# Kernel optimization log

Hardware: AMD Instinct MI355X
Metric: run time of the kernel (lower is better)

Reference implementation:

```python
import jax, jax.numpy as jnp
import numpy as np

C = 256
GROUPS = 32
EPS = 1e-5


def setup_inputs() -> dict:
    key = jax.random.key(0)
    ks = jax.random.split(key, 7)
    B, D, H, W = 2, 8, 48, 48
    x = jax.random.normal(ks[0], (B, C, D, H, W), dtype=jnp.float32)
    norm_w = jnp.ones((C,), jnp.float32)
    norm_b = jnp.zeros((C,), jnp.float32)
    qkv_w = jax.random.normal(ks[1], (3 * C, C), jnp.float32) * (1.0 / np.sqrt(C))
    qkv_b = jnp.zeros((3 * C,), jnp.float32)
    proj_w = jax.random.normal(ks[2], (C, C), jnp.float32) * (1.0 / np.sqrt(C))
    proj_b = jnp.zeros((C,), jnp.float32)
    return {"x": x, "norm_w": norm_w, "norm_b": norm_b,
            "qkv_w": qkv_w, "qkv_b": qkv_b,
            "proj_w": proj_w, "proj_b": proj_b}


def _group_norm(x, w, b):
    B, Cc, D, H, Wd = x.shape
    xg = x.reshape(B, GROUPS, Cc // GROUPS, D, H, Wd)
    mu = xg.mean(axis=(2, 3, 4, 5), keepdims=True)
    var = xg.var(axis=(2, 3, 4, 5), keepdims=True)
    xn = ((xg - mu) * jax.lax.rsqrt(var + EPS)).reshape(B, Cc, D, H, Wd)
    return xn * w[None, :, None, None, None] + b[None, :, None, None, None]


def reference(x, norm_w, norm_b, qkv_w, qkv_b, proj_w, proj_b):
    Cc = x.shape[1]
    h = _group_norm(x, norm_w, norm_b)
    # 1x1x1 conv == channel matmul
    qkv = jnp.einsum('oc,bcdhw->bodhw', qkv_w, h) + qkv_b[None, :, None, None, None]
    q, k, v = jnp.split(qkv, 3, axis=1)
    scale = (Cc // 8) ** (-0.5)
    # [B, D, h, w, H, W] dense spatial attention per depth slice
    attn = jnp.einsum('bcdhw,bcdHW->bdhwHW', q * scale, k)
    # NOTE: original code softmaxes over the LAST axis only (W), not (H,W) jointly.
    attn = jax.nn.softmax(attn, axis=-1)
    out = jnp.einsum('bdhwHW,bcdHW->bcdhw', attn, v)
    out = jnp.einsum('oc,bcdhw->bodhw', proj_w, out) + proj_b[None, :, None, None, None]
    return x + out
```

## Files before the change

kernel.cpp:

```cpp
#include <hip/hip_runtime.h>
#include <hip/hip_bf16.h>

typedef __attribute__((ext_vector_type(8))) short short8;
typedef __attribute__((ext_vector_type(4))) float f32x4;
typedef __attribute__((ext_vector_type(16))) float f32x16;
typedef __attribute__((ext_vector_type(4))) unsigned int u32x4;
typedef unsigned int u32;
typedef unsigned short u16;

#define C_ 256
#define G_ 32
#define ND_ 18432
#define HW_ 2304
#define EPS_ 1e-5f
#define QS2_ 0.25503487f

static __device__ __forceinline__ u16 f2bf(float f) {
  __hip_bfloat16 h = __float2bfloat16(f);
  return __builtin_bit_cast(u16, h);
}

static __device__ __forceinline__ void gll16(const void* g, void* l) {
  __builtin_amdgcn_global_load_lds(
      (const __attribute__((address_space(1))) unsigned int*)g,
      (__attribute__((address_space(3))) unsigned int*)l, 16, 0, 0);
}

__global__ void k_convert_w(const float* __restrict__ qkv_w,
                            const float* __restrict__ proj_w,
                            u16* __restrict__ wout,
                            float* __restrict__ raw) {
  if (blockIdx.x == 0 && threadIdx.x < 128) raw[threadIdx.x] = 0.f;
  int i = blockIdx.x * 256 + threadIdx.x;
  if (i < 196608) wout[i] = f2bf(qkv_w[i]);
  else            wout[i] = f2bf(proj_w[i - 196608]);
}

__global__ __launch_bounds__(256) void k_gn_part(const float* __restrict__ x,
                                                 float* __restrict__ raw) {
  int grp = blockIdx.x >> 2, sub = blockIdx.x & 3;
  const float4* p = (const float4*)(x + (size_t)grp * 147456 + sub * 36864);
  float s1 = 0.f, s2 = 0.f;
  for (int i = threadIdx.x; i < 9216; i += 256) {
    float4 v = p[i];
    s1 += v.x + v.y + v.z + v.w;
    s2 += v.x*v.x + v.y*v.y + v.z*v.z + v.w*v.w;
  }
  for (int off = 1; off < 64; off <<= 1) {
    s1 += __shfl_xor(s1, off, 64);
    s2 += __shfl_xor(s2, off, 64);
  }
  __shared__ float a1[4], a2[4];
  int w = threadIdx.x >> 6;
  if ((threadIdx.x & 63) == 0) { a1[w] = s1; a2[w] = s2; }
  __syncthreads();
  if (threadIdx.x == 0) {
    float t1 = a1[0] + a1[1] + a1[2] + a1[3];
    float t2 = a2[0] + a2[1] + a2[2] + a2[3];
    atomicAdd(&raw[grp * 2], t1);
    atomicAdd(&raw[grp * 2 + 1], t2);
  }
}

__global__ void k_gn_fin(const float* __restrict__ raw, float* __restrict__ stats) {
  int g = threadIdx.x;
  if (g < 64) {
    float mu  = raw[g * 2] / 147456.0f;
    float var = raw[g * 2 + 1] / 147456.0f - mu * mu;
    stats[g * 2]     = mu;
    stats[g * 2 + 1] = rsqrtf(var + EPS_);
  }
}

__global__ __launch_bounds__(256) void k_tnorm(const float* __restrict__ x,
                                               const float* __restrict__ stats,
                                               const float* __restrict__ nw,
                                               const float* __restrict__ nb,
                                               u16* __restrict__ h_t) {
  __shared__ u16 tl[64 * 66];
  int wg = blockIdx.x;
  int nt = wg % 288; int ct = (wg / 288) & 3; int b = wg / 1152;
  int c0 = ct * 64, n0 = nt * 64;
  int tid = threadIdx.x;
#pragma unroll
  for (int p = 0; p < 4; p++) {
    int c_l = p * 16 + (tid >> 4);
    int n4  = (tid & 15) * 4;
    int cg  = c0 + c_l;
    float4 v = *(const float4*)(x + ((size_t)(b * C_ + cg)) * ND_ + n0 + n4);
    float mu = stats[(b * G_ + (cg >> 3)) * 2];
    float rs = stats[(b * G_ + (cg >> 3)) * 2 + 1];
    float w = nw[cg], bia = nb[cg];
    tl[(n4 + 0) * 66 + c_l] = f2bf((v.x - mu) * rs * w + bia);
    tl[(n4 + 1) * 66 + c_l] = f2bf((v.y - mu) * rs * w + bia);
    tl[(n4 + 2) * 66 + c_l] = f2bf((v.z - mu) * rs * w + bia);
    tl[(n4 + 3) * 66 + c_l] = f2bf((v.w - mu) * rs * w + bia);
  }
  __syncthreads();
#pragma unroll
  for (int p = 0; p < 2; p++) {
    int idx = p * 256 + tid;
    int n_l = idx >> 3, c8 = idx & 7;
    const u32* s = (const u32*)((const char*)tl + n_l * 132 + c8 * 16);
    uint4 vv; vv.x = s[0]; vv.y = s[1]; vv.z = s[2]; vv.w = s[3];
    *(uint4*)(h_t + ((size_t)(b * ND_ + n0 + n_l)) * C_ + c0 + c8 * 8) = vv;
  }
}

__global__ __launch_bounds__(256) void k_qk(const u16* __restrict__ h_t,
                                            const u16* __restrict__ w_qkv,
                                            const float* __restrict__ qkv_b,
                                            u16* __restrict__ q_ws,
                                            u16* __restrict__ k_ws) {
  int wg = blockIdx.x;
  int nt = wg % 288; int ot = (wg / 288) & 3; int b = wg / 1152;
  int n0 = nt * 64, o0 = ot * 128;
  int lane = threadIdx.x & 63; int w = threadIdx.x >> 6;
  int g = lane >> 4, lid = lane & 15;
  int n_w = n0 + w * 16;
  f32x4 acc[8];
#pragma unroll
  for (int t = 0; t < 8; t++) acc[t] = (f32x4){0.f, 0.f, 0.f, 0.f};
  const short8* Ab = (const short8*)(h_t + ((size_t)(b * ND_ + n_w + lid)) * C_ + g * 8);
#pragma unroll
  for (int ks = 0; ks < 8; ks++) {
    short8 a = Ab[ks * 4];
#pragma unroll
    for (int t = 0; t < 8; t++) {
      short8 bf = *(const short8*)(w_qkv + ((size_t)(o0 + t * 16 + lid)) * C_ + ks * 32 + g * 8);
      acc[t] = __builtin_amdgcn_mfma_f32_16x16x32_bf16(a, bf, acc[t], 0, 0, 0);
    }
  }
  if (o0 < 256) {
#pragma unroll
    for (int t = 0; t < 8; t++) {
      int o_t = o0 + t * 16;
      float bias = qkv_b[o_t + lid];
#pragma unroll
      for (int r = 0; r < 4; r++) {
        int n_idx = n_w + g * 4 + r;
        q_ws[((size_t)(b * ND_ + n_idx)) * C_ + o_t + lid] = f2bf((acc[t][r] + bias) * QS2_);
      }
    }
  } else {
#pragma unroll
    for (int t = 0; t < 8; t++) {
      int o_t = o0 + t * 16;
      float bias = qkv_b[o_t + lid];
      int oc = o_t - 256 + lid;
#pragma unroll
      for (int r = 0; r < 4; r++) {
        int n_idx = n_w + g * 4 + r;
        int dd = n_idx / 2304, hw = n_idx % 2304;
        int tt = hw / 48, kk = hw % 48;
        size_t off = ((size_t)((b * 8 + dd) * 48 + tt) * 1536 + (oc >> 3) * 48 + kk) * 8 + (oc & 7);
        k_ws[off] = f2bf(acc[t][r] + bias);
      }
    }
  }
}

__global__ __launch_bounds__(256) void k_v(const u16* __restrict__ h_t,
                                           const u16* __restrict__ w_qkv,
                                           const float* __restrict__ qkv_b,
                                           u16* __restrict__ v_ws) {
  int wg = blockIdx.x;
  int nt = wg % 144; int ot = (wg / 144) & 3; int b = wg / 576;
  int n0 = nt * 128, o0 = ot * 64;
  int lane = threadIdx.x & 63; int w = threadIdx.x >> 6;
  int g = lane >> 4, lid = lane & 15;
  int o_w = o0 + w * 16;
  f32x4 acc[8];
#pragma unroll
  for (int t = 0; t < 8; t++) acc[t] = (f32x4){0.f, 0.f, 0.f, 0.f};
  const short8* Ab = (const short8*)(w_qkv + ((size_t)(512 + o_w + lid)) * C_ + g * 8);
#pragma unroll
  for (int ks = 0; ks < 8; ks++) {
    short8 a = Ab[ks * 4];
#pragma unroll
    for (int t = 0; t < 8; t++) {
      short8 bf = *(const short8*)(h_t + ((size_t)(b * ND_ + n0 + t * 16 + lid)) * C_ + ks * 32 + g * 8);
      acc[t] = __builtin_amdgcn_mfma_f32_16x16x32_bf16(a, bf, acc[t], 0, 0, 0);
    }
  }
#pragma unroll
  for (int t = 0; t < 8; t++) {
#pragma unroll
    for (int r = 0; r < 4; r++) {
      int o = o_w + g * 4 + r;
      int n = n0 + t * 16 + lid;
      int d = n / 2304; int hw = n % 2304;
      int grp = hw / 48; int j = hw % 48;
      size_t idx = ((size_t)(((b * 8 + d) * 48 + grp) * 6 + (j >> 3))) * 2048 + o * 8 + (j & 7);
      v_ws[idx] = f2bf(acc[t][r] + qkv_b[512 + o]);
    }
  }
}

__global__ __launch_bounds__(256, 2) void k_attn(const u16* __restrict__ q_ws,
                                                 const u16* __restrict__ k_ws,
                                                 const u16* __restrict__ v_ws,
                                                 u16* __restrict__ ao) {
  __shared__ __align__(16) unsigned char lds[74240];
  int wg = blockIdx.x;
  int virt = (wg & 7) * 36 + (wg >> 3);
  int slice = virt / 18;
  int qt = virt % 18;
  int b = slice >> 3, d = slice & 7;
  int tid = threadIdx.x;
  int lane = tid & 63, w = tid >> 6;
  int l31 = lane & 31, hi = lane >> 5;

  const char* kgb = (const char*)k_ws + (size_t)slice * 1179648;
  const char* vgb = (const char*)v_ws + (size_t)slice * 1179648;

  size_t nbase = (size_t)b * ND_ + d * HW_ + qt * 128 + w * 32;
  const char* qp = (const char*)q_ws + (nbase + l31) * 512 + hi * 16;
  short8 qf[16];
#pragma unroll
  for (int ks = 0; ks < 16; ks++) qf[ks] = *(const short8*)(qp + ks * 32);

  f32x16 acc[8];
#pragma unroll
  for (int i = 0; i < 8; i++) acc[i] = (f32x16)0.0f;

#define STG_K(t_, base_) {                                             \
    const char* s_ = kgb + (size_t)(t_) * 24576 + tid * 16;            \
    char* d_ = (char*)lds + (base_) + w * 1024;                        \
    _Pragma("unroll")                                                  \
    for (int i_ = 0; i_ < 6; i_++)                                     \
      gll16(s_ + i_ * 4096, d_ + i_ * 4096);                           \
  }
#define STG_V(t_) {                                                    \
    const char* s_ = vgb + (size_t)(t_) * 24576 + tid * 16;            \
    char* d_ = (char*)lds + 49152 + w * 1024;                          \
    _Pragma("unroll")                                                  \
    for (int i_ = 0; i_ < 6; i_++)                                     \
      gll16(s_ + i_ * 4096, d_ + i_ * 4096);                           \
  }

  STG_K(0, 0);
  STG_V(0);
  __builtin_amdgcn_sched_barrier(0);
  asm volatile("s_waitcnt vmcnt(0)" ::: "memory");
  __builtin_amdgcn_sched_barrier(0);
  __builtin_amdgcn_s_barrier();

  int kcur = 0;
  for (int t = 0; t < 48; t++) {
    if (t < 47) STG_K(t + 1, (kcur ^ 1) * 24576);

    const char* kb = (const char*)lds + kcur * 24576;

    f32x16 S0 = (f32x16)0.0f, S1 = (f32x16)0.0f;
#pragma unroll
    for (int ks = 0; ks < 16; ks++) {
      const char* p = kb + (ks * 2 + hi) * 768 + l31 * 16;
      short8 k0 = *(const short8*)(p);
      short8 k1 = *(const short8*)(p + 512);
      S0 = __builtin_amdgcn_mfma_f32_32x32x16_bf16(k0, qf[ks], S0, 0, 0, 0);
      S1 = __builtin_amdgcn_mfma_f32_32x32x16_bf16(k1, qf[ks], S1, 0, 0, 0);
    }

#pragma unroll
    for (int r = 0; r < 16; r++) S0[r] = __builtin_amdgcn_exp2f(S0[r]);
#pragma unroll
    for (int r = 0; r < 8; r++)  S1[r] = __builtin_amdgcn_exp2f(S1[r]);
    float z = 0.f;
#pragma unroll
    for (int r = 0; r < 16; r++) z += S0[r];
#pragma unroll
    for (int r = 0; r < 8; r++)  z += S1[r];
    z += __shfl_xor(z, 32, 64);
    float inv = __builtin_amdgcn_rcpf(z);
#pragma unroll
    for (int r = 0; r < 16; r++) S0[r] *= inv;
#pragma unroll
    for (int r = 0; r < 8; r++)  S1[r] *= inv;

    short8 pa[3];
#pragma unroll
    for (int s = 0; s < 3; s++) {
      const f32x16& P = (s < 2) ? S0 : S1;
      const int a = (s == 1) ? 8 : 0;
      u32 u0, u1, v0, v1;
      asm("v_cvt_pk_bf16_f32 %0, %1, %2" : "=v"(u0) : "v"(P[a + 0]), "v"(P[a + 1]));
      asm("v_cvt_pk_bf16_f32 %0, %1, %2" : "=v"(u1) : "v"(P[a + 2]), "v"(P[a + 3]));
      asm("v_cvt_pk_bf16_f32 %0, %1, %2" : "=v"(v0) : "v"(P[a + 4]), "v"(P[a + 5]));
      asm("v_cvt_pk_bf16_f32 %0, %1, %2" : "=v"(v1) : "v"(P[a + 6]), "v"(P[a + 7]));
      asm("v_permlane32_swap_b32 %0, %1" : "+v"(u0), "+v"(v0));
      asm("v_permlane32_swap_b32 %0, %1" : "+v"(u1), "+v"(v1));
      u32x4 wv; wv[0] = u0; wv[1] = u1; wv[2] = v0; wv[3] = v1;
      pa[s] = __builtin_bit_cast(short8, wv);
    }

    __builtin_amdgcn_sched_barrier(0);
    asm volatile("s_waitcnt vmcnt(0)" ::: "memory");
    __builtin_amdgcn_sched_barrier(0);
    __builtin_amdgcn_s_barrier();

    const char* vb = (const char*)lds + 49152;
#pragma unroll
    for (int s = 0; s < 3; s++) {
      const char* vs = vb + (s * 2 + hi) * 4096 + l31 * 16;
#pragma unroll
      for (int ct = 0; ct < 8; ct++) {
        short8 vf = *(const short8*)(vs + ct * 512);
        acc[ct] = __builtin_amdgcn_mfma_f32_32x32x16_bf16(pa[s], vf, acc[ct], 0, 0, 0);
      }
    }

    __builtin_amdgcn_s_barrier();
    if (t < 47) STG_V(t + 1);
    kcur ^= 1;
  }

#pragma unroll
  for (int ct = 0; ct < 8; ct++) {
#pragma unroll
    for (int r = 0; r < 16; r++) {
      int ql = (r & 3) + 8 * (r >> 2) + 4 * hi;
      ao[(nbase + ql) * 256 + ct * 32 + l31] = f2bf(acc[ct][r]);
    }
  }
}

__global__ __launch_bounds__(256) void k_proj(const u16* __restrict__ ao,
                                              const u16* __restrict__ w_p,
                                              const float* __restrict__ proj_b,
                                              const float* __restrict__ x,
                                              float* __restrict__ out) {
  int wg = blockIdx.x;
  int nt = wg % 144; int ot = (wg / 144) & 3; int b = wg / 576;
  int n0 = nt * 128, o0 = ot * 64;
  int lane = threadIdx.x & 63; int w = threadIdx.x >> 6;
  int g = lane >> 4, lid = lane & 15;
  int o_w = o0 + w * 16;
  f32x4 acc[8];
#pragma unroll
  for (int t = 0; t < 8; t++) acc[t] = (f32x4){0.f, 0.f, 0.f, 0.f};
  const short8* Ab = (const short8*)(w_p + ((size_t)(o_w + lid)) * C_ + g * 8);
#pragma unroll
  for (int ks = 0; ks < 8; ks++) {
    short8 a = Ab[ks * 4];
#pragma unroll
    for (int t = 0; t < 8; t++) {
      short8 bf = *(const short8*)(ao + ((size_t)(b * ND_ + n0 + t * 16 + lid)) * C_ + ks * 32 + g * 8);
      acc[t] = __builtin_amdgcn_mfma_f32_16x16x32_bf16(a, bf, acc[t], 0, 0, 0);
    }
  }
#pragma unroll
  for (int t = 0; t < 8; t++) {
#pragma unroll
    for (int r = 0; r < 4; r++) {
      int o = o_w + g * 4 + r;
      size_t off = ((size_t)(b * C_ + o)) * ND_ + n0 + t * 16 + lid;
      out[off] = acc[t][r] + proj_b[o] + x[off];
    }
  }
}

extern "C" void kernel_launch(void* const* d_in, const int* in_sizes, int n_in,
                              void* d_out, int out_size, void* d_ws, size_t ws_size,
                              hipStream_t stream) {
  const float* x      = (const float*)d_in[0];
  const float* norm_w = (const float*)d_in[1];
  const float* norm_b = (const float*)d_in[2];
  const float* qkv_w  = (const float*)d_in[3];
  const float* qkv_b  = (const float*)d_in[4];
  const float* proj_w = (const float*)d_in[5];
  const float* proj_b = (const float*)d_in[6];

  char* ws = (char*)d_ws;
  float* stats = (float*)ws;
  float* raw   = (float*)(ws + 512);
  u16* w_qkv = (u16*)(ws + 1024);
  u16* w_p   = (u16*)(ws + 1024 + 393216);
  u16* h_t   = (u16*)(ws + 525312);
  u16* q_ws  = h_t + 9437184;
  u16* k_ws  = q_ws + 9437184;
  u16* v_ws  = k_ws + 9437184;
  u16* ao    = h_t;
  float* out = (float*)d_out;

  if (ws_size < (size_t)525312 + 4ull * 9437184ull * 2ull) return;

  hipLaunchKernelGGL(k_convert_w, dim3(1024), dim3(256), 0, stream, qkv_w, proj_w, w_qkv, raw);
  hipLaunchKernelGGL(k_gn_part,   dim3(256),  dim3(256), 0, stream, x, raw);
  hipLaunchKernelGGL(k_gn_fin,    dim3(1),    dim3(64),  0, stream, raw, stats);
  hipLaunchKernelGGL(k_tnorm,     dim3(2304), dim3(256), 0, stream, x, stats, norm_w, norm_b, h_t);
  hipLaunchKernelGGL(k_qk,        dim3(2304), dim3(256), 0, stream, h_t, w_qkv, qkv_b, q_ws, k_ws);
  hipLaunchKernelGGL(k_v,         dim3(1152), dim3(256), 0, stream, h_t, w_qkv, qkv_b, v_ws);
  hipLaunchKernelGGL(k_attn,      dim3(288),  dim3(256), 0, stream, q_ws, k_ws, v_ws, ao);
  hipLaunchKernelGGL(k_proj,      dim3(1152), dim3(256), 0, stream, ao, w_p, proj_b, x, out);
}
```

Baseline: 335.4 us.

## Process two query tiles per wave in attention to reuse K/V staging

Each wave in the attention kernel now computes two 32-row query tiles against each staged K/V tile, so each workgroup covers 256 queries and the grid halves from 288 to 144 blocks. Every K and V fragment read from LDS feeds twice as many MFMAs, and total global K/V staging traffic is halved. The cost is doubled accumulator and Q register use, which forces occupancy down to one block per CU. With 144 blocks on a 256-CU part, many CUs sit idle, trading parallelism for reuse.

```diff
diff --git a/kernel.cpp b/kernel.cpp
--- a/kernel.cpp
+++ b/kernel.cpp
@@ -197,15 +197,15 @@
   }
 }
 
-__global__ __launch_bounds__(256, 2) void k_attn(const u16* __restrict__ q_ws,
+__global__ __launch_bounds__(256, 1) void k_attn(const u16* __restrict__ q_ws,
                                                  const u16* __restrict__ k_ws,
                                                  const u16* __restrict__ v_ws,
                                                  u16* __restrict__ ao) {
-  __shared__ __align__(16) unsigned char lds[74240];
+  __shared__ __align__(16) unsigned char lds[84480];
   int wg = blockIdx.x;
-  int virt = (wg & 7) * 36 + (wg >> 3);
-  int slice = virt / 18;
-  int qt = virt % 18;
+  int virt = (wg & 7) * 18 + (wg >> 3);
+  int slice = virt / 9;
+  int qt = virt % 9;
   int b = slice >> 3, d = slice & 7;
   int tid = threadIdx.x;
   int lane = tid & 63, w = tid >> 6;
@@ -214,15 +214,17 @@
   const char* kgb = (const char*)k_ws + (size_t)slice * 1179648;
   const char* vgb = (const char*)v_ws + (size_t)slice * 1179648;
 
-  size_t nbase = (size_t)b * ND_ + d * HW_ + qt * 128 + w * 32;
-  const char* qp = (const char*)q_ws + (nbase + l31) * 512 + hi * 16;
-  short8 qf[16];
-#pragma unroll
-  for (int ks = 0; ks < 16; ks++) qf[ks] = *(const short8*)(qp + ks * 32);
-
-  f32x16 acc[8];
-#pragma unroll
-  for (int i = 0; i < 8; i++) acc[i] = (f32x16)0.0f;
+  size_t nbase = (size_t)b * ND_ + d * HW_ + qt * 256 + w * 64;
+  const char* qpA = (const char*)q_ws + (nbase + l31) * 512 + hi * 16;
+  const char* qpB = qpA + 32 * 512;
+  short8 qfa[16], qfb[16];
+#pragma unroll
+  for (int ks = 0; ks < 16; ks++) { qfa[ks] = *(const short8*)(qpA + ks * 32);
+                                    qfb[ks] = *(const short8*)(qpB + ks * 32); }
+
+  f32x16 accA[8], accB[8];
+#pragma unroll
+  for (int i = 0; i < 8; i++) { accA[i] = (f32x16)0.0f; accB[i] = (f32x16)0.0f; }
 
 #define STG_K(t_, base_) {                                             \
     const char* s_ = kgb + (size_t)(t_) * 24576 + tid * 16;            \
@@ -252,46 +254,54 @@
 
     const char* kb = (const char*)lds + kcur * 24576;
 
-    f32x16 S0 = (f32x16)0.0f, S1 = (f32x16)0.0f;
+    f32x16 S0a = (f32x16)0.0f, S1a = (f32x16)0.0f;
+    f32x16 S0b = (f32x16)0.0f, S1b = (f32x16)0.0f;
 #pragma unroll
     for (int ks = 0; ks < 16; ks++) {
       const char* p = kb + (ks * 2 + hi) * 768 + l31 * 16;
       short8 k0 = *(const short8*)(p);
       short8 k1 = *(const short8*)(p + 512);
-      S0 = __builtin_amdgcn_mfma_f32_32x32x16_bf16(k0, qf[ks], S0, 0, 0, 0);
-      S1 = __builtin_amdgcn_mfma_f32_32x32x16_bf16(k1, qf[ks], S1, 0, 0, 0);
-    }
-
-#pragma unroll
-    for (int r = 0; r < 16; r++) S0[r] = __builtin_amdgcn_exp2f(S0[r]);
-#pragma unroll
-    for (int r = 0; r < 8; r++)  S1[r] = __builtin_amdgcn_exp2f(S1[r]);
-    float z = 0.f;
-#pragma unroll
-    for (int r = 0; r < 16; r++) z += S0[r];
-#pragma unroll
-    for (int r = 0; r < 8; r++)  z += S1[r];
-    z += __shfl_xor(z, 32, 64);
-    float inv = __builtin_amdgcn_rcpf(z);
-#pragma unroll
-    for (int r = 0; r < 16; r++) S0[r] *= inv;
-#pragma unroll
-    for (int r = 0; r < 8; r++)  S1[r] *= inv;
-
-    short8 pa[3];
-#pragma unroll
-    for (int s = 0; s < 3; s++) {
-      const f32x16& P = (s < 2) ? S0 : S1;
-      const int a = (s == 1) ? 8 : 0;
-      u32 u0, u1, v0, v1;
-      asm("v_cvt_pk_bf16_f32 %0, %1, %2" : "=v"(u0) : "v"(P[a + 0]), "v"(P[a + 1]));
-      asm("v_cvt_pk_bf16_f32 %0, %1, %2" : "=v"(u1) : "v"(P[a + 2]), "v"(P[a + 3]));
-      asm("v_cvt_pk_bf16_f32 %0, %1, %2" : "=v"(v0) : "v"(P[a + 4]), "v"(P[a + 5]));
-      asm("v_cvt_pk_bf16_f32 %0, %1, %2" : "=v"(v1) : "v"(P[a + 6]), "v"(P[a + 7]));
-      asm("v_permlane32_swap_b32 %0, %1" : "+v"(u0), "+v"(v0));
-      asm("v_permlane32_swap_b32 %0, %1" : "+v"(u1), "+v"(v1));
-      u32x4 wv; wv[0] = u0; wv[1] = u1; wv[2] = v0; wv[3] = v1;
-      pa[s] = __builtin_bit_cast(short8, wv);
+      S0a = __builtin_amdgcn_mfma_f32_32x32x16_bf16(k0, qfa[ks], S0a, 0, 0, 0);
+      S0b = __builtin_amdgcn_mfma_f32_32x32x16_bf16(k0, qfb[ks], S0b, 0, 0, 0);
+      S1a = __builtin_amdgcn_mfma_f32_32x32x16_bf16(k1, qfa[ks], S1a, 0, 0, 0);
+      S1b = __builtin_amdgcn_mfma_f32_32x32x16_bf16(k1, qfb[ks], S1b, 0, 0, 0);
+    }
+
+    short8 paA[3], paB[3];
+#pragma unroll
+    for (int tile = 0; tile < 2; tile++) {
+      f32x16& S0 = tile ? S0b : S0a;
+      f32x16& S1 = tile ? S1b : S1a;
+#pragma unroll
+      for (int r = 0; r < 16; r++) S0[r] = __builtin_amdgcn_exp2f(S0[r]);
+#pragma unroll
+      for (int r = 0; r < 8; r++)  S1[r] = __builtin_amdgcn_exp2f(S1[r]);
+      float z = 0.f;
+#pragma unroll
+      for (int r = 0; r < 16; r++) z += S0[r];
+#pragma unroll
+      for (int r = 0; r < 8; r++)  z += S1[r];
+      z += __shfl_xor(z, 32, 64);
+      float inv = __builtin_amdgcn_rcpf(z);
+#pragma unroll
+      for (int r = 0; r < 16; r++) S0[r] *= inv;
+#pragma unroll
+      for (int r = 0; r < 8; r++)  S1[r] *= inv;
+      short8* pa = tile ? paB : paA;
+#pragma unroll
+      for (int s = 0; s < 3; s++) {
+        const f32x16& P = (s < 2) ? S0 : S1;
+        const int a = (s == 1) ? 8 : 0;
+        u32 u0, u1, v0, v1;
+        asm("v_cvt_pk_bf16_f32 %0, %1, %2" : "=v"(u0) : "v"(P[a + 0]), "v"(P[a + 1]));
+        asm("v_cvt_pk_bf16_f32 %0, %1, %2" : "=v"(u1) : "v"(P[a + 2]), "v"(P[a + 3]));
+        asm("v_cvt_pk_bf16_f32 %0, %1, %2" : "=v"(v0) : "v"(P[a + 4]), "v"(P[a + 5]));
+        asm("v_cvt_pk_bf16_f32 %0, %1, %2" : "=v"(v1) : "v"(P[a + 6]), "v"(P[a + 7]));
+        asm("v_permlane32_swap_b32 %0, %1" : "+v"(u0), "+v"(v0));
+        asm("v_permlane32_swap_b32 %0, %1" : "+v"(u1), "+v"(v1));
+        u32x4 wv; wv[0] = u0; wv[1] = u1; wv[2] = v0; wv[3] = v1;
+        pa[s] = __builtin_bit_cast(short8, wv);
+      }
     }
 
     __builtin_amdgcn_sched_barrier(0);
@@ -306,7 +316,8 @@
 #pragma unroll
       for (int ct = 0; ct < 8; ct++) {
         short8 vf = *(const short8*)(vs + ct * 512);
-        acc[ct] = __builtin_amdgcn_mfma_f32_32x32x16_bf16(pa[s], vf, acc[ct], 0, 0, 0);
+        accA[ct] = __builtin_amdgcn_mfma_f32_32x32x16_bf16(paA[s], vf, accA[ct], 0, 0, 0);
+        accB[ct] = __builtin_amdgcn_mfma_f32_32x32x16_bf16(paB[s], vf, accB[ct], 0, 0, 0);
       }
     }
 
@@ -320,7 +331,8 @@
 #pragma unroll
     for (int r = 0; r < 16; r++) {
       int ql = (r & 3) + 8 * (r >> 2) + 4 * hi;
-      ao[(nbase + ql) * 256 + ct * 32 + l31] = f2bf(acc[ct][r]);
+      ao[(nbase + ql) * 256 + ct * 32 + l31]      = f2bf(accA[ct][r]);
+      ao[(nbase + 32 + ql) * 256 + ct * 32 + l31] = f2bf(accB[ct][r]);
     }
   }
 }
@@ -391,6 +403,6 @@
   hipLaunchKernelGGL(k_tnorm,     dim3(2304), dim3(256), 0, stream, x, stats, norm_w, norm_b, h_t);
   hipLaunchKernelGGL(k_qk,        dim3(2304), dim3(256), 0, stream, h_t, w_qkv, qkv_b, q_ws, k_ws);
   hipLaunchKernelGGL(k_v,         dim3(1152), dim3(256), 0, stream, h_t, w_qkv, qkv_b, v_ws);
-  hipLaunchKernelGGL(k_attn,      dim3(288),  dim3(256), 0, stream, q_ws, k_ws, v_ws, ao);
+  hipLaunchKernelGGL(k_attn,      dim3(144),  dim3(256), 0, stream, q_ws, k_ws, v_ws, ao);
   hipLaunchKernelGGL(k_proj,      dim3(1152), dim3(256), 0, stream, ao, w_p, proj_b, x, out);
 }
```

After: 369.8 us. 10.3% more time.
